# Kernel tuning notes

Measured on AMD Instinct MI355X. Metric: run time of the kernel, lower is better.

The kernel has to match this reference:

```python
import jax, jax.numpy as jnp
import numpy as np

B, OBS, H, M, L1, T, A = 16384, 376, 512, 8, 3, 50, 17  # L1 = num_layers - 1
LOG_SQRT_2PI = 0.5 * np.log(2.0 * np.pi).astype(np.float32)


def setup_inputs() -> dict:
    key = jax.random.key(0)
    ks = jax.random.split(key, 16)
    s = lambda fan: 1.0 / np.sqrt(fan).astype(np.float32)
    return {
        "x": jax.random.normal(ks[0], (B, OBS), jnp.float32),
        "task_idx": jax.random.randint(ks[1], (B,), 0, T, jnp.int64),
        "enc_W1": jax.random.normal(ks[2], (OBS, H), jnp.float32) * s(OBS),
        "enc_b1": jnp.zeros((H,), jnp.float32),
        "enc_W2": jax.random.normal(ks[3], (H, H), jnp.float32) * s(H),
        "enc_b2": jnp.zeros((H,), jnp.float32),
        "task_emb": jax.random.normal(ks[4], (T, H), jnp.float32),
        "a_rW": jax.random.normal(ks[5], (L1, H, M * M), jnp.float32) * s(H),
        "a_rb": jnp.zeros((L1, M * M), jnp.float32),
        "c_rW": jax.random.normal(ks[6], (L1, H, M * M), jnp.float32) * s(H),
        "c_rb": jnp.zeros((L1, M * M), jnp.float32),
        "a_W": jax.random.normal(ks[7], (L1, M, H, H), jnp.float32) * s(H),
        "a_b": jnp.zeros((L1, M, H), jnp.float32),
        "a_Wf": jax.random.normal(ks[8], (M, H, A), jnp.float32) * 0.01,
        "a_bf": jnp.zeros((M, A), jnp.float32),
        "c_W": jax.random.normal(ks[9], (L1, M, H, H), jnp.float32) * s(H),
        "c_b": jnp.zeros((L1, M, H), jnp.float32),
        "c_Wf": jax.random.normal(ks[10], (M, H, 1), jnp.float32) * s(H),
        "c_bf": jnp.zeros((M, 1), jnp.float32),
        "actor_logstd": jnp.zeros((1, A), jnp.float32),
    }


def _routing(context, rW, rb):
    # context: [B,H]; rW: [L1,H,M*M] -> list of [B,M,M] softmax routing probs
    rel = jax.nn.relu(context)
    probs = []
    for l in range(L1):
        logits = (rel @ rW[l] + rb[l]).reshape(-1, M, M)
        probs.append(jax.nn.softmax(logits, axis=2))
    return probs


def _base(f_s, probs, W, b, Wf, bf):
    # f_s: [B,H]; W: [L1,M,H,H]; Wf: [M,H,out]
    g = jnp.broadcast_to(f_s[:, None, :], (f_s.shape[0], M, H))  # [B,M,H]
    for l in range(L1):
        outs = jax.nn.relu(jnp.einsum("bmh,mhk->bmk", g, W[l]) + b[l])  # [B,M,H]
        g = jnp.einsum("bij,bjh->bih", probs[l], outs)  # soft combine
    final = jnp.einsum("bmh,mhk->bmk", g, Wf) + bf  # [B,M,out]
    return final.sum(axis=1)


def reference(x, task_idx, enc_W1, enc_b1, enc_W2, enc_b2, task_emb,
              a_rW, a_rb, c_rW, c_rb, a_W, a_b, a_Wf, a_bf,
              c_W, c_b, c_Wf, c_bf, actor_logstd):
    f_s = jnp.tanh(jnp.tanh(x @ enc_W1 + enc_b1) @ enc_W2 + enc_b2)  # [B,H]
    h_z = task_emb[task_idx]  # [B,H]
    context = f_s * h_z

    value = _base(f_s, _routing(context, c_rW, c_rb), c_W, c_b, c_Wf, c_bf)  # [B,1]
    mean = _base(f_s, _routing(context, a_rW, a_rb), a_W, a_b, a_Wf, a_bf)   # [B,A]

    # deterministic action (sample=False): action = mean
    logstd = jnp.broadcast_to(actor_logstd, mean.shape)
    log_prob = (-logstd - LOG_SQRT_2PI).sum(axis=1)          # N.log_prob(mean).sum(1)
    entropy = (0.5 + LOG_SQRT_2PI + logstd).sum(axis=1)
    # concat (action, log_prob, entropy, value) -> [B, A+3]
    return jnp.concatenate([mean, log_prob[:, None], entropy[:, None], value], axis=1)
```

## Files before the change

### kernel.cpp

```cpp
#include <hip/hip_runtime.h>
#include <hip/hip_bf16.h>

typedef float f32x4 __attribute__((ext_vector_type(4)));
typedef float f32x2 __attribute__((ext_vector_type(2)));
typedef int   i32x4 __attribute__((ext_vector_type(4)));
typedef int   i32x8 __attribute__((ext_vector_type(8)));

#define LOG_SQRT_2PI 0.91893853320467274f

static constexpr int BSZ  = 16384;
static constexpr int OBSN = 376;
static constexpr int HD   = 512;
static constexpr int NACT = 17;

__device__ __forceinline__ unsigned char f2fp8(float v) {
  return (unsigned char)(__builtin_amdgcn_cvt_pk_fp8_f32(v, v, 0, false) & 0xFF);
}

__device__ __forceinline__ void gl16(const unsigned char* g, unsigned char* l) {
  __builtin_amdgcn_global_load_lds((const __attribute__((address_space(1))) void*)g,
                                   (__attribute__((address_space(3))) void*)l, 16, 0, 0);
}

__device__ __forceinline__ void xcd_map(int id, int gx, int gy, int& bx, int& by, int& bz) {
  int p = id & 7, l = id >> 3;
  bx = l % gx;
  int g = (l / gx) * 8 + p;
  by = g % gy;
  bz = g / gy;
}


__global__ void k_cvt_pad8(const float* __restrict__ src, unsigned char* __restrict__ dst) {
  long i = (long)blockIdx.x * 256 + threadIdx.x;
  if (i >= (long)BSZ * HD) return;
  long r = i >> 9;
  int  c = (int)(i & 511);
  dst[i] = f2fp8(c < OBSN ? src[r * OBSN + c] : 0.f);
}

__global__ void k_packT8(const float* __restrict__ src, unsigned char* __restrict__ dst,
                         int K, int N, int Kpad, long sstride, long dstride, float scale) {
  __shared__ float t[32][33];
  src += (long)blockIdx.z * sstride;
  dst += (long)blockIdx.z * dstride;
  int k0 = blockIdx.y * 32, n0 = blockIdx.x * 32;
#pragma unroll
  for (int ii = 0; ii < 4; ++ii) {
    int i = ii * 8 + threadIdx.y;
    int k = k0 + i, n = n0 + threadIdx.x;
    t[i][threadIdx.x] = (k < K && n < N) ? src[(long)k * N + n] : 0.f;
  }
  __syncthreads();
#pragma unroll
  for (int ii = 0; ii < 4; ++ii) {
    int i = ii * 8 + threadIdx.y;
    int n = n0 + i, k = k0 + threadIdx.x;
    if (n < N && k < Kpad) dst[(long)n * Kpad + k] = f2fp8(scale * t[threadIdx.x][i]);
  }
}

__global__ void k_packwF(const float* __restrict__ aW, const float* __restrict__ cW,
                         unsigned char* __restrict__ dst) {
  long i = (long)blockIdx.x * 256 + threadIdx.x;
  if (i >= (long)48 * 262144) return;
  int z = (int)(i >> 18);
  int rem = (int)(i & 262143);
  int k = rem >> 9, n = rem & 511;
  int layer = z >> 4, zz = z & 15, net = zz >> 3, m = zz & 7;
  const float* src = (net ? aW : cW) + (long)(layer * 8 + m) * 262144;
  float v = src[(long)k * 512 + n];
  int t = k >> 7, nb = n >> 4;
  int lane = ((k >> 5) & 3) * 16 + (n & 15);
  long off = ((((long)z * 4 + t) * 32 + nb) * 64 + lane) * 32 + (k & 31);
  dst[off] = f2fp8(16.f * v);
}

__global__ void k_packmisc(const float* __restrict__ a_b, const float* __restrict__ c_b,
                           const float* __restrict__ aWf, const float* __restrict__ cWf,
                           const float* __restrict__ a_rb, const float* __restrict__ c_rb,
                           float* __restrict__ lb, unsigned char* __restrict__ dsta,
                           unsigned char* __restrict__ dstc, float* __restrict__ rb) {
  int i = blockIdx.x * 256 + threadIdx.x;
  if (i < 24576) {
    int layer = i >> 13, zz = (i >> 9) & 15, n = i & 511;
    int net = zz >> 3, m = zz & 7;
    lb[i] = (net ? a_b : c_b)[(layer * 8 + m) * 512 + n];
  } else if (i < 24576 + 131072) {
    int j = i - 24576;
    int n = j >> 12, kn = j & 4095;
    int hb = kn >> 9, rem = kn & 511, m = rem >> 6, u = kn & 63;
    int ko = m * 512 + hb * 64 + u;
    dsta[j] = (n < NACT) ? f2fp8(64.f * aWf[(long)ko * NACT + n]) : (unsigned char)0;
    dstc[j] = (n < 1)    ? f2fp8(64.f * cWf[ko])                  : (unsigned char)0;
  } else if (i < 24576 + 131072 + 384) {
    int j = i - 24576 - 131072;
    rb[j] = (j < 192) ? a_rb[j] : c_rb[j - 192];
  }
}

__global__ void k_initout2(const float* __restrict__ a_bf, const float* __restrict__ c_bf,
                           const float* __restrict__ ls, float* __restrict__ out) {
  long i = (long)blockIdx.x * 256 + threadIdx.x;
  if (i >= (long)BSZ * 20) return;
  int o = (int)(i % 20);
  float v = 0.f;
  if (o < NACT) {
    for (int m = 0; m < 8; ++m) v += a_bf[m * NACT + o];
  } else if (o == 19) {
    for (int m = 0; m < 8; ++m) v += c_bf[m];
  } else if (o == 17) {
    for (int a = 0; a < NACT; ++a) v += -ls[a] - LOG_SQRT_2PI;
  } else {
    for (int a = 0; a < NACT; ++a) v += 0.5f + LOG_SQRT_2PI + ls[a];
  }
  out[i] = v;
}

template <int OP>
__global__ __launch_bounds__(256, 4)
void k_gemm8(const unsigned char* __restrict__ A, const unsigned char* __restrict__ Bt,
             void* __restrict__ Cv, const float* __restrict__ bias,
             int N, int K, int lda, int ldc, int gx, int gy,
             const int* __restrict__ tidx, const float* __restrict__ temb,
             unsigned char* __restrict__ out2) {
  __shared__ alignas(16) unsigned char sA[128 * 128];
  __shared__ alignas(16) unsigned char sB[128 * 128];
  int bx, by, z;
  xcd_map(blockIdx.x, gx, gy, bx, by, z);
  const int tid  = threadIdx.x;
  const int wave = tid >> 6, lane = tid & 63;
  const int wr = (wave >> 1) * 64, wc = (wave & 1) * 64;
  const int row0 = by * 128, col0 = bx * 128;
  const int lcol = lane & 15, quad = lane >> 4;
  const int sw7 = lcol & 7;
  const int c0 = ((2 * quad)     ^ sw7) * 16;
  const int c1 = ((2 * quad + 1) ^ sw7) * 16;
  const int raA0 = (wr + lcol) * 128 + c0, raA1 = (wr + lcol) * 128 + c1;
  const int rbB0 = (wc + lcol) * 128 + c0, rbB1 = (wc + lcol) * 128 + c1;
  int aOff[4], bOff[4];
#pragma unroll
  for (int i = 0; i < 4; ++i) {
    int u = i * 256 + tid;
    int r = u >> 3, gc = (u & 7) ^ (r & 7);
    aOff[i] = (row0 + r) * lda + gc * 16;
    bOff[i] = (col0 + r) * K + gc * 16;
  }

  f32x4 acc[4][4] = {};

  for (int kt = 0; kt < K; kt += 128) {
#pragma unroll
    for (int i = 0; i < 4; ++i) gl16(A + aOff[i] + kt, &sA[i * 4096 + tid * 16]);
#pragma unroll
    for (int i = 0; i < 4; ++i) gl16(Bt + bOff[i] + kt, &sB[i * 4096 + tid * 16]);
    __syncthreads();
    i32x8 bv[4];
#pragma unroll
    for (int ni = 0; ni < 4; ++ni) {
      i32x4 blo = *(const i32x4*)&sB[rbB0 + ni * 2048];
      i32x4 bhi = *(const i32x4*)&sB[rbB1 + ni * 2048];
      bv[ni] = (i32x8){blo[0], blo[1], blo[2], blo[3], bhi[0], bhi[1], bhi[2], bhi[3]};
    }
#pragma unroll
    for (int mi = 0; mi < 4; ++mi) {
      i32x4 alo = *(const i32x4*)&sA[raA0 + mi * 2048];
      i32x4 ahi = *(const i32x4*)&sA[raA1 + mi * 2048];
      i32x8 af = (i32x8){alo[0], alo[1], alo[2], alo[3], ahi[0], ahi[1], ahi[2], ahi[3]};
#pragma unroll
      for (int ni = 0; ni < 4; ++ni)
        acc[mi][ni] = __builtin_amdgcn_mfma_scale_f32_16x16x128_f8f6f4(
            bv[ni], af, acc[mi][ni], 0, 0, 0, 0x7F, 0, 0x7F);
    }
    __syncthreads();
  }

#pragma unroll
  for (int ni = 0; ni < 4; ++ni) {
    int colb = col0 + wc + ni * 16 + quad * 4;
    if (colb >= N) continue;
    float4 bw = *(const float4*)&bias[colb];
#pragma unroll
    for (int mi = 0; mi < 4; ++mi) {
      int rowg = row0 + wr + mi * 16 + lcol;
      float v0 = acc[mi][ni][0] * 0.0625f + bw.x;
      float v1 = acc[mi][ni][1] * 0.0625f + bw.y;
      float v2 = acc[mi][ni][2] * 0.0625f + bw.z;
      float v3 = acc[mi][ni][3] * 0.0625f + bw.w;
      long idx = (long)rowg * ldc + colb;
      if (OP == 1) {
        float t0 = tanhf(v0), t1 = tanhf(v1), t2 = tanhf(v2), t3 = tanhf(v3);
        unsigned d = __builtin_amdgcn_cvt_pk_fp8_f32(t0, t1, 0, false);
        d = __builtin_amdgcn_cvt_pk_fp8_f32(t2, t3, d, true);
        *(unsigned*)&((unsigned char*)Cv)[idx] = d;
      } else if (OP == 5) {
        float t0 = tanhf(v0), t1 = tanhf(v1), t2 = tanhf(v2), t3 = tanhf(v3);
        unsigned d = __builtin_amdgcn_cvt_pk_fp8_f32(t0, t1, 0, false);
        d = __builtin_amdgcn_cvt_pk_fp8_f32(t2, t3, d, true);
        *(unsigned*)&((unsigned char*)Cv)[idx] = d;
        int tk = tidx[rowg];
        float4 te = *(const float4*)&temb[(long)tk * HD + colb];
        unsigned e = __builtin_amdgcn_cvt_pk_fp8_f32(fmaxf(t0 * te.x, 0.f), fmaxf(t1 * te.y, 0.f), 0, false);
        e = __builtin_amdgcn_cvt_pk_fp8_f32(fmaxf(t2 * te.z, 0.f), fmaxf(t3 * te.w, 0.f), e, true);
        *(unsigned*)&out2[idx] = e;
      } else if (OP == 4) {
        float mx = fmaxf(fmaxf(v0, v1), fmaxf(v2, v3));
        mx = fmaxf(mx, __shfl_xor(mx, 16));
        float e0 = __expf(v0 - mx), e1 = __expf(v1 - mx), e2 = __expf(v2 - mx), e3 = __expf(v3 - mx);
        float s = e0 + e1 + e2 + e3;
        s += __shfl_xor(s, 16);
        float inv = 1.f / s;
        *(float4*)&((float*)Cv)[idx] = make_float4(e0 * inv, e1 * inv, e2 * inv, e3 * inv);
      }
    }
  }
}

template <int AMODE, int HEAD>
__global__ __launch_bounds__(512, 4)
void k_gemmF(const unsigned char* __restrict__ A, const unsigned char* __restrict__ Wp,
             const float* __restrict__ lb, const float* __restrict__ probs,
             unsigned char* __restrict__ g, int gy, int poffC, int poffA,
             const unsigned char* __restrict__ Wfc, const unsigned char* __restrict__ Wfa,
             float* __restrict__ outp) {
  __shared__ alignas(16) unsigned char sL[AMODE ? 65536 : 32768];
  int hb, slab, net;
  xcd_map(blockIdx.x, 8, gy, hb, slab, net);
  const int tid = threadIdx.x;
  const int w = tid >> 6, lane = tid & 63;
  const int lcol = lane & 15, quad = lane >> 4;
  const int ln3 = lane >> 3, sl = lane & 7;
  const int row0 = slab * 64;
  const int h0 = hb * 64;
  const int sw7 = lcol & 7;
  const int c0 = ((2 * quad)     ^ sw7) * 16;
  const int c1 = ((2 * quad + 1) ^ sw7) * 16;
  const int ch = sl ^ ln3;
  const unsigned char* wbase =
      Wp + (((long)(net * 8 + w) * 4 * 32 + hb * 4) * 64 + lane) * 32;

  f32x4 acc[4][4] = {};

  if (AMODE == 0) {
#pragma unroll
    for (int i = 0; i < 4; ++i) {
      int vb = w * 4 + i;
      int rr = (vb & 7) * 8 + ln3;
      gl16(A + (row0 + rr) * 512 + (vb >> 3) * 128 + ch * 16, &sL[(vb * 64 + lane) * 16]);
    }
    __syncthreads();
#pragma unroll
    for (int t = 0; t < 4; ++t) {
      i32x8 bv[4];
#pragma unroll
      for (int ni = 0; ni < 4; ++ni) {
        i32x4 lo = *(const i32x4*)(wbase + t * 65536 + ni * 2048);
        i32x4 hi = *(const i32x4*)(wbase + t * 65536 + ni * 2048 + 16);
        bv[ni] = (i32x8){lo[0], lo[1], lo[2], lo[3], hi[0], hi[1], hi[2], hi[3]};
      }
#pragma unroll
      for (int mi = 0; mi < 4; ++mi) {
        int ra = t * 8192 + (mi * 16 + lcol) * 128;
        i32x4 lo = *(const i32x4*)&sL[ra + c0];
        i32x4 hi = *(const i32x4*)&sL[ra + c1];
        i32x8 af = (i32x8){lo[0], lo[1], lo[2], lo[3], hi[0], hi[1], hi[2], hi[3]};
#pragma unroll
        for (int ni = 0; ni < 4; ++ni)
          acc[mi][ni] = __builtin_amdgcn_mfma_scale_f32_16x16x128_f8f6f4(
              bv[ni], af, acc[mi][ni], 0, 0, 0, 0x7F, 0, 0x7F);
      }
    }
  } else {
    const unsigned char* abase = A + (long)(row0 + ln3) * 8192 + net * 4096 +
                                 w * 64 + (ch >> 2) * 512 + (ch & 3) * 16;
    unsigned char* dbase = &sL[w * 8192 + lane * 16];
#pragma unroll 1
    for (int t = 0; t < 4; ++t) {
#pragma unroll
      for (int i = 0; i < 8; ++i)
        gl16(abase + i * 8 * 8192 + t * 1024, dbase + i * 1024);
      i32x8 bv[4];
#pragma unroll
      for (int ni = 0; ni < 4; ++ni) {
        i32x4 lo = *(const i32x4*)(wbase + t * 65536 + ni * 2048);
        i32x4 hi = *(const i32x4*)(wbase + t * 65536 + ni * 2048 + 16);
        bv[ni] = (i32x8){lo[0], lo[1], lo[2], lo[3], hi[0], hi[1], hi[2], hi[3]};
      }
      asm volatile("s_waitcnt vmcnt(0)" ::: "memory");
      __builtin_amdgcn_sched_barrier(0);
#pragma unroll
      for (int mi = 0; mi < 4; ++mi) {
        int ra = w * 8192 + (mi * 16 + lcol) * 128;
        i32x4 lo = *(const i32x4*)&sL[ra + c0];
        i32x4 hi = *(const i32x4*)&sL[ra + c1];
        i32x8 af = (i32x8){lo[0], lo[1], lo[2], lo[3], hi[0], hi[1], hi[2], hi[3]};
#pragma unroll
        for (int ni = 0; ni < 4; ++ni)
          acc[mi][ni] = __builtin_amdgcn_mfma_scale_f32_16x16x128_f8f6f4(
              bv[ni], af, acc[mi][ni], 0, 0, 0, 0x7F, 0, 0x7F);
      }
    }
  }

  __syncthreads();

#pragma unroll
  for (int ni = 0; ni < 4; ++ni) {
    int col = ni * 16 + quad * 4;
    float4 bw = *(const float4*)&lb[(net * 8 + w) * 512 + h0 + col];
    int sd = ni * 4 + quad;
#pragma unroll
    for (int mi = 0; mi < 4; ++mi) {
      int row = mi * 16 + lcol;
      float v0 = fmaxf(acc[mi][ni][0] * 0.0625f + bw.x, 0.f);
      float v1 = fmaxf(acc[mi][ni][1] * 0.0625f + bw.y, 0.f);
      float v2 = fmaxf(acc[mi][ni][2] * 0.0625f + bw.z, 0.f);
      float v3 = fmaxf(acc[mi][ni][3] * 0.0625f + bw.w, 0.f);
      unsigned d = __builtin_amdgcn_cvt_pk_fp8_f32(v0, v1, 0, false);
      d = __builtin_amdgcn_cvt_pk_fp8_f32(v2, v3, d, true);
      *(unsigned*)&sL[w * 4096 + row * 64 + ((sd ^ (row & 14)) << 2)] = d;
    }
  }
  __syncthreads();

  const int poff = net ? poffA : poffC;
#pragma unroll
  for (int k = 0; k < 8; ++k) {
    const int r = k * 8 + ln3;
    const float* pr = &probs[(long)(row0 + r) * 384 + poff + w * 8];
    float4 pA = *(const float4*)pr;
    float4 pB = *(const float4*)(pr + 4);
    float p8[8] = {pA.x, pA.y, pA.z, pA.w, pB.x, pB.y, pB.z, pB.w};
    f32x2 ga2[4] = {};
#pragma unroll
    for (int j = 0; j < 8; ++j) {
      uint2 o2 = *(const uint2*)&sL[j * 4096 + r * 64 + (((sl * 2) ^ (r & 14)) << 2)];
      f32x2 pw2 = {p8[j], p8[j]};
      ga2[0] += pw2 * __builtin_amdgcn_cvt_pk_f32_fp8(o2.x, false);
      ga2[1] += pw2 * __builtin_amdgcn_cvt_pk_f32_fp8(o2.x, true);
      ga2[2] += pw2 * __builtin_amdgcn_cvt_pk_f32_fp8(o2.y, false);
      ga2[3] += pw2 * __builtin_amdgcn_cvt_pk_f32_fp8(o2.y, true);
    }
    unsigned lo = __builtin_amdgcn_cvt_pk_fp8_f32(ga2[0][0], ga2[0][1], 0, false);
    lo = __builtin_amdgcn_cvt_pk_fp8_f32(ga2[1][0], ga2[1][1], lo, true);
    unsigned hi = __builtin_amdgcn_cvt_pk_fp8_f32(ga2[2][0], ga2[2][1], 0, false);
    hi = __builtin_amdgcn_cvt_pk_fp8_f32(ga2[3][0], ga2[3][1], hi, true);
    if (HEAD) {
      *(uint2*)&sL[32768 + w * 4096 + r * 64 + (((sl * 2) ^ (r & 14)) << 2)] =
          make_uint2(lo, hi);
    } else {
      *(uint2*)&g[(long)(row0 + r) * 8192 + net * 4096 + hb * 512 + w * 64 + sl * 8] =
          make_uint2(lo, hi);
    }
  }

  if (HEAD) {
    __syncthreads();
    const unsigned char* Wf = net ? Wfa : Wfc;
    const int ooff = net ? 0 : 19;
    const int mi = w & 3, kh = w >> 2;
    const int hrow = mi * 16 + lcol;
    f32x4 hacc[2] = {};
#pragma unroll
    for (int ks = 0; ks < 8; ++ks) {
      int j = kh * 4 + (ks >> 1);
      int u = (ks & 1) * 32 + quad * 8;
      int sd = u >> 2;
      long af = *(const long*)&sL[32768 + j * 4096 + hrow * 64 + ((sd ^ (hrow & 14)) << 2)];
      int kglob = hb * 512 + kh * 256 + ks * 32 + quad * 8;
      long bv0 = *(const long*)&Wf[(long)lcol * 4096 + kglob];
      hacc[0] = __builtin_amdgcn_mfma_f32_16x16x32_fp8_fp8(af, bv0, hacc[0], 0, 0, 0);
      if (net) {
        long bv1 = *(const long*)&Wf[(long)(16 + lcol) * 4096 + kglob];
        hacc[1] = __builtin_amdgcn_mfma_f32_16x16x32_fp8_fp8(af, bv1, hacc[1], 0, 0, 0);
      }
    }
    const int NOUTn = net ? NACT : 1;
#pragma unroll
    for (int ni = 0; ni < 2; ++ni) {
      if (ni == 1 && !net) break;
      int col = ni * 16 + lcol;
      if (col >= NOUTn) continue;
#pragma unroll
      for (int rr = 0; rr < 4; ++rr) {
        int row = row0 + mi * 16 + quad * 4 + rr;
        atomicAdd(&outp[(long)row * 20 + ooff + col], hacc[ni][rr] * 0.015625f);
      }
    }
  }
}


extern "C" void kernel_launch(void* const* d_in, const int* in_sizes, int n_in,
                              void* d_out, int out_size, void* d_ws, size_t ws_size,
                              hipStream_t stream) {
  const float* x        = (const float*)d_in[0];
  const int*   task_idx = (const int*)d_in[1];
  const float* enc_W1   = (const float*)d_in[2];
  const float* enc_b1   = (const float*)d_in[3];
  const float* enc_W2   = (const float*)d_in[4];
  const float* enc_b2   = (const float*)d_in[5];
  const float* task_emb = (const float*)d_in[6];
  const float* a_rW     = (const float*)d_in[7];
  const float* a_rb     = (const float*)d_in[8];
  const float* c_rW     = (const float*)d_in[9];
  const float* c_rb     = (const float*)d_in[10];
  const float* a_W      = (const float*)d_in[11];
  const float* a_b      = (const float*)d_in[12];
  const float* a_Wf     = (const float*)d_in[13];
  const float* a_bf     = (const float*)d_in[14];
  const float* c_W      = (const float*)d_in[15];
  const float* c_b      = (const float*)d_in[16];
  const float* c_Wf     = (const float*)d_in[17];
  const float* c_bf     = (const float*)d_in[18];
  const float* logstd   = (const float*)d_in[19];
  float* out = (float*)d_out;

  char* ws = (char*)d_ws;
  size_t off = 0;
  auto carve = [&](size_t bytes) {
    char* p = ws + off;
    off += (bytes + 255) & ~(size_t)255;
    return p;
  };
  unsigned char* W8 = (unsigned char*)carve((size_t)48 * 262144);
  unsigned char* W1T8 = (unsigned char*)carve((size_t)512 * 512);
  unsigned char* W2T8 = (unsigned char*)carve((size_t)512 * 512);
  unsigned char* rWT8 = (unsigned char*)carve((size_t)384 * 512);
  float* rball = (float*)carve(384 * 4);
  float* lb    = (float*)carve(3 * 16 * 512 * 4);
  unsigned char* WfaT8 = (unsigned char*)carve((size_t)32 * 4096);
  unsigned char* WfcT8 = (unsigned char*)carve((size_t)32 * 4096);
  unsigned char* fs8 = (unsigned char*)carve((size_t)BSZ * HD);
  float* lgt   = (float*)carve((size_t)BSZ * 384 * 4);

  size_t remain = (ws_size > off) ? (ws_size - off) : 0;
  int Bc = 2048;
  for (int cand = BSZ; cand > 2048; cand >>= 1)
    if ((size_t)2 * cand * 8192 <= remain) { Bc = cand; break; }
  size_t half = (size_t)Bc * 8192;
  unsigned char* bufA8 = (unsigned char*)carve(half);
  unsigned char* bufB8 = (unsigned char*)carve(half);
  unsigned char* x8   = bufA8;
  unsigned char* h18  = bufB8;
  unsigned char* rel8 = bufA8;

  dim3 tb(32, 8);

  k_cvt_pad8<<<(int)(((long)BSZ * HD + 255) / 256), 256, 0, stream>>>(x, x8);
  k_packT8<<<dim3(16, 16, 1), tb, 0, stream>>>(enc_W1, W1T8, OBSN, 512, 512, 0, 0, 16.f);
  k_packT8<<<dim3(16, 16, 1), tb, 0, stream>>>(enc_W2, W2T8, 512, 512, 512, 0, 0, 16.f);
  k_packT8<<<dim3(2, 16, 3),  tb, 0, stream>>>(a_rW, rWT8,             512, 64, 512, 512 * 64, 64 * 512, 16.f);
  k_packT8<<<dim3(2, 16, 3),  tb, 0, stream>>>(c_rW, rWT8 + 192 * 512, 512, 64, 512, 512 * 64, 64 * 512, 16.f);
  k_packwF<<<(int)(((long)48 * 262144 + 255) / 256), 256, 0, stream>>>(a_W, c_W, W8);
  k_packmisc<<<610, 256, 0, stream>>>(a_b, c_b, a_Wf, c_Wf, a_rb, c_rb,
                                      lb, WfaT8, WfcT8, rball);
  k_initout2<<<(int)(((long)BSZ * 20 + 255) / 256), 256, 0, stream>>>(a_bf, c_bf, logstd, out);

  const int GY = BSZ / 128;
  k_gemm8<1><<<4 * GY, 256, 0, stream>>>(x8, W1T8, h18, enc_b1, 512, 512, 512, 512,
                                         4, GY, nullptr, nullptr, nullptr);
  k_gemm8<5><<<4 * GY, 256, 0, stream>>>(h18, W2T8, fs8, enc_b2, 512, 512, 512, 512,
                                         4, GY, task_idx, task_emb, rel8);
  k_gemm8<4><<<3 * GY, 256, 0, stream>>>(rel8, rWT8, lgt, rball, 384, 512, 512, 384,
                                         3, GY, nullptr, nullptr, nullptr);

  const size_t wlz = (size_t)16 * 262144;
  for (int c0 = 0; c0 < BSZ; c0 += Bc) {
    const unsigned char* fs_c = fs8 + (long)c0 * 512;
    const float* pr_c  = lgt + (long)c0 * 384;
    float*       out_c = out + (long)c0 * 20;
    const int gyF = Bc / 64;

    k_gemmF<0, 0><<<16 * gyF, 512, 0, stream>>>(fs_c, W8, lb, pr_c, bufA8, gyF, 192, 0,
                                                nullptr, nullptr, nullptr);
    k_gemmF<1, 0><<<16 * gyF, 512, 0, stream>>>(bufA8, W8 + wlz, lb + 8192, pr_c, bufB8,
                                                gyF, 192 + 64, 64, nullptr, nullptr, nullptr);
    k_gemmF<1, 1><<<16 * gyF, 512, 0, stream>>>(bufB8, W8 + 2 * wlz, lb + 16384, pr_c, bufA8,
                                                gyF, 192 + 128, 128, WfcT8, WfaT8, out_c);
  }
}
```

Baseline: 725.7 us.

## Tile weight packing through LDS and halve LDS staging in routed GEMM

The fp8 weight-packing kernel now stages 128x128 tiles in shared memory and writes the packed layout with 16-byte vector stores, replacing scattered per-byte stores. In the routed-combine GEMM path (AMODE=1), the A operand is loaded in two halves of 4 rows per wave. This halves that path's LDS footprint to 32KB unless HEAD needs 64KB, aiming for higher occupancy. MFMA sections are wrapped in s_setprio to favour matrix issue. The split adds extra waits that serialize the second load behind the first compute half.

```diff
diff --git a/kernel.cpp b/kernel.cpp
--- a/kernel.cpp
+++ b/kernel.cpp
@@ -62,18 +62,34 @@
 
 __global__ void k_packwF(const float* __restrict__ aW, const float* __restrict__ cW,
                          unsigned char* __restrict__ dst) {
-  long i = (long)blockIdx.x * 256 + threadIdx.x;
-  if (i >= (long)48 * 262144) return;
-  int z = (int)(i >> 18);
-  int rem = (int)(i & 262143);
-  int k = rem >> 9, n = rem & 511;
-  int layer = z >> 4, zz = z & 15, net = zz >> 3, m = zz & 7;
+  __shared__ unsigned char sT[128 * 144];
+  const int tid = threadIdx.x;
+  const int z = blockIdx.z;
+  const int t = blockIdx.y;
+  const int ng = blockIdx.x;
+  const int layer = z >> 4, zz = z & 15, net = zz >> 3, m = zz & 7;
   const float* src = (net ? aW : cW) + (long)(layer * 8 + m) * 262144;
-  float v = src[(long)k * 512 + n];
-  int t = k >> 7, nb = n >> 4;
-  int lane = ((k >> 5) & 3) * 16 + (n & 15);
-  long off = ((((long)z * 4 + t) * 32 + nb) * 64 + lane) * 32 + (k & 31);
-  dst[off] = f2fp8(16.f * v);
+#pragma unroll
+  for (int i = 0; i < 64; ++i) {
+    int lin = i * 256 + tid;
+    int kl = lin >> 7, nl = lin & 127;
+    float v = src[(long)(t * 128 + kl) * 512 + ng * 128 + nl];
+    sT[nl * 144 + kl] = f2fp8(16.f * v);
+  }
+  __syncthreads();
+#pragma unroll
+  for (int f = 0; f < 2; ++f) {
+    int fid = f * 256 + tid;
+    int lane = fid & 63, nb_l = fid >> 6;
+    int n_l = nb_l * 16 + (lane & 15);
+    int klo = ((lane >> 4) & 3) * 32;
+    uint4 lo = *(const uint4*)&sT[n_l * 144 + klo];
+    uint4 hi = *(const uint4*)&sT[n_l * 144 + klo + 16];
+    int nb = ng * 8 + nb_l;
+    unsigned char* d = dst + ((((long)z * 4 + t) * 32 + nb) * 64 + lane) * 32;
+    *(uint4*)d = lo;
+    *(uint4*)(d + 16) = hi;
+  }
 }
 
 __global__ void k_packmisc(const float* __restrict__ a_b, const float* __restrict__ c_b,
@@ -223,7 +239,7 @@
              unsigned char* __restrict__ g, int gy, int poffC, int poffA,
              const unsigned char* __restrict__ Wfc, const unsigned char* __restrict__ Wfa,
              float* __restrict__ outp) {
-  __shared__ alignas(16) unsigned char sL[AMODE ? 65536 : 32768];
+  __shared__ alignas(16) unsigned char sL[HEAD ? 65536 : 32768];
   int hb, slab, net;
   xcd_map(blockIdx.x, 8, gy, hb, slab, net);
   const int tid = threadIdx.x;
@@ -258,6 +274,7 @@
         i32x4 hi = *(const i32x4*)(wbase + t * 65536 + ni * 2048 + 16);
         bv[ni] = (i32x8){lo[0], lo[1], lo[2], lo[3], hi[0], hi[1], hi[2], hi[3]};
       }
+      __builtin_amdgcn_s_setprio(1);
 #pragma unroll
       for (int mi = 0; mi < 4; ++mi) {
         int ra = t * 8192 + (mi * 16 + lcol) * 128;
@@ -269,15 +286,16 @@
           acc[mi][ni] = __builtin_amdgcn_mfma_scale_f32_16x16x128_f8f6f4(
               bv[ni], af, acc[mi][ni], 0, 0, 0, 0x7F, 0, 0x7F);
       }
+      __builtin_amdgcn_s_setprio(0);
     }
   } else {
     const unsigned char* abase = A + (long)(row0 + ln3) * 8192 + net * 4096 +
                                  w * 64 + (ch >> 2) * 512 + (ch & 3) * 16;
-    unsigned char* dbase = &sL[w * 8192 + lane * 16];
+    unsigned char* dbase = &sL[w * 4096 + lane * 16];
 #pragma unroll 1
     for (int t = 0; t < 4; ++t) {
 #pragma unroll
-      for (int i = 0; i < 8; ++i)
+      for (int i = 0; i < 4; ++i)
         gl16(abase + i * 8 * 8192 + t * 1024, dbase + i * 1024);
       i32x8 bv[4];
 #pragma unroll
@@ -288,9 +306,10 @@
       }
       asm volatile("s_waitcnt vmcnt(0)" ::: "memory");
       __builtin_amdgcn_sched_barrier(0);
-#pragma unroll
-      for (int mi = 0; mi < 4; ++mi) {
-        int ra = w * 8192 + (mi * 16 + lcol) * 128;
+      __builtin_amdgcn_s_setprio(1);
+#pragma unroll
+      for (int mi = 0; mi < 2; ++mi) {
+        int ra = w * 4096 + (mi * 16 + lcol) * 128;
         i32x4 lo = *(const i32x4*)&sL[ra + c0];
         i32x4 hi = *(const i32x4*)&sL[ra + c1];
         i32x8 af = (i32x8){lo[0], lo[1], lo[2], lo[3], hi[0], hi[1], hi[2], hi[3]};
@@ -298,6 +317,31 @@
         for (int ni = 0; ni < 4; ++ni)
           acc[mi][ni] = __builtin_amdgcn_mfma_scale_f32_16x16x128_f8f6f4(
               bv[ni], af, acc[mi][ni], 0, 0, 0, 0x7F, 0, 0x7F);
+      }
+      __builtin_amdgcn_s_setprio(0);
+      asm volatile("s_waitcnt lgkmcnt(0)" ::: "memory");
+      __builtin_amdgcn_sched_barrier(0);
+#pragma unroll
+      for (int i = 0; i < 4; ++i)
+        gl16(abase + (i + 4) * 8 * 8192 + t * 1024, dbase + i * 1024);
+      asm volatile("s_waitcnt vmcnt(0)" ::: "memory");
+      __builtin_amdgcn_sched_barrier(0);
+      __builtin_amdgcn_s_setprio(1);
+#pragma unroll
+      for (int mi = 2; mi < 4; ++mi) {
+        int ra = w * 4096 + ((mi - 2) * 16 + lcol) * 128;
+        i32x4 lo = *(const i32x4*)&sL[ra + c0];
+        i32x4 hi = *(const i32x4*)&sL[ra + c1];
+        i32x8 af = (i32x8){lo[0], lo[1], lo[2], lo[3], hi[0], hi[1], hi[2], hi[3]};
+#pragma unroll
+        for (int ni = 0; ni < 4; ++ni)
+          acc[mi][ni] = __builtin_amdgcn_mfma_scale_f32_16x16x128_f8f6f4(
+              bv[ni], af, acc[mi][ni], 0, 0, 0, 0x7F, 0, 0x7F);
+      }
+      __builtin_amdgcn_s_setprio(0);
+      if (t < 3) {
+        asm volatile("s_waitcnt lgkmcnt(0)" ::: "memory");
+        __builtin_amdgcn_sched_barrier(0);
       }
     }
   }
@@ -452,7 +496,7 @@
   k_packT8<<<dim3(16, 16, 1), tb, 0, stream>>>(enc_W2, W2T8, 512, 512, 512, 0, 0, 16.f);
   k_packT8<<<dim3(2, 16, 3),  tb, 0, stream>>>(a_rW, rWT8,             512, 64, 512, 512 * 64, 64 * 512, 16.f);
   k_packT8<<<dim3(2, 16, 3),  tb, 0, stream>>>(c_rW, rWT8 + 192 * 512, 512, 64, 512, 512 * 64, 64 * 512, 16.f);
-  k_packwF<<<(int)(((long)48 * 262144 + 255) / 256), 256, 0, stream>>>(a_W, c_W, W8);
+  k_packwF<<<dim3(4, 4, 48), 256, 0, stream>>>(a_W, c_W, W8);
   k_packmisc<<<610, 256, 0, stream>>>(a_b, c_b, a_Wf, c_Wf, a_rb, c_rb,
                                       lb, WfaT8, WfcT8, rball);
   k_initout2<<<(int)(((long)BSZ * 20 + 255) / 256), 256, 0, stream>>>(a_bf, c_bf, logstd, out);
```

Result: slower. 803.7 us (+10.7%).
